# Optimization experiments

Measured on AMD Instinct MI355X. Metric: run time of the kernel, lower is better.

Reference implementation:

```python
import jax, jax.numpy as jnp
import numpy as np

V, E, H, D = 32000, 512, 512, 512  # vocab, emb_dim, enc_hid_dim, dec_hid_dim
B, S, T = 32, 64, 48               # batch, src_len, trg_len


def _gru_cell(x, h, Wih, Whh, bih, bhh):
    # PyTorch GRU cell semantics (gate order r, z, n)
    gi = x @ Wih.T + bih
    gh = h @ Whh.T + bhh
    ir, iz, i_n = jnp.split(gi, 3, axis=-1)
    hr, hz, h_n = jnp.split(gh, 3, axis=-1)
    r = jax.nn.sigmoid(ir + hr)
    z = jax.nn.sigmoid(iz + hz)
    n = jnp.tanh(i_n + r * h_n)
    return (1.0 - z) * n + z * h


def setup_inputs() -> dict:
    key = jax.random.key(0)
    ks = jax.random.split(key, 21)
    f = lambda k, shp: jax.random.normal(k, shp, dtype=jnp.float32) * 0.05
    inp = {
        'src': jax.random.randint(ks[0], (B, S), 0, V),
        'trg': jax.random.randint(ks[1], (T, B), 0, V),
        'emb': f(ks[2], (V, E)),
        'encf_Wih': f(ks[3], (3 * H, E)), 'encf_Whh': f(ks[4], (3 * H, H)),
        'encf_bih': f(ks[5], (3 * H,)), 'encf_bhh': f(ks[6], (3 * H,)),
        'encb_Wih': f(ks[7], (3 * H, E)), 'encb_Whh': f(ks[8], (3 * H, H)),
        'encb_bih': f(ks[9], (3 * H,)), 'encb_bhh': f(ks[10], (3 * H,)),
        'fc_W': f(ks[11], (D, 2 * H)), 'fc_b': f(ks[12], (D,)),
        'attn_W': f(ks[13], (D, D + 2 * H)), 'attn_v': f(ks[14], (D,)),
        'dec_Wih': f(ks[15], (3 * D, E + 2 * H)), 'dec_Whh': f(ks[16], (3 * D, D)),
        'dec_bih': f(ks[17], (3 * D,)), 'dec_bhh': f(ks[18], (3 * D,)),
        'out_W': f(ks[19], (V, 2 * H + D + E)),
        'out_b': jnp.zeros((V,), dtype=jnp.float32),
    }
    return inp


def _forward(src, trg, emb, encf_Wih, encf_Whh, encf_bih, encf_bhh,
             encb_Wih, encb_Whh, encb_bih, encb_bhh, fc_W, fc_b,
             attn_W, attn_v, dec_Wih, dec_Whh, dec_bih, dec_bhh, out_W, out_b):
    x = emb[src]                       # [B,S,E]
    xT = jnp.swapaxes(x, 0, 1)         # [S,B,E]
    h0 = jnp.zeros((src.shape[0], encf_Whh.shape[1]), dtype=x.dtype)

    def stepf(h, xt):
        h2 = _gru_cell(xt, h, encf_Wih, encf_Whh, encf_bih, encf_bhh)
        return h2, h2

    def stepb(h, xt):
        h2 = _gru_cell(xt, h, encb_Wih, encb_Whh, encb_bih, encb_bhh)
        return h2, h2

    hf, yf = jax.lax.scan(stepf, h0, xT)
    hb, yb = jax.lax.scan(stepb, h0, xT[::-1])
    # [B,S,2H] bidirectional encoder outputs (backward stream re-reversed)
    enc_out = jnp.concatenate([jnp.swapaxes(yf, 0, 1), jnp.swapaxes(yb[::-1], 0, 1)], axis=-1)
    # decoder init state from final fwd/bwd hidden
    s0 = jnp.tanh(jnp.concatenate([hf, hb], axis=-1) @ fc_W.T + fc_b)  # [B,D]

    def dec_step(s, tok):
        e = emb[tok]  # [B,E]
        srep = jnp.broadcast_to(s[:, None, :], (s.shape[0], enc_out.shape[1], s.shape[1]))
        energy = jnp.tanh(jnp.concatenate([srep, enc_out], axis=-1) @ attn_W.T)  # [B,S,D]
        a = jax.nn.softmax(energy @ attn_v, axis=1)  # [B,S]
        c = jnp.einsum('bs,bsh->bh', a, enc_out)     # [B,2H]
        s2 = _gru_cell(jnp.concatenate([e, c], axis=-1), s, dec_Wih, dec_Whh, dec_bih, dec_bhh)
        pred = jnp.concatenate([s2, c, e], axis=-1) @ out_W.T + out_b  # [B,V]
        return s2, pred

    # teacher forcing: decoder inputs are trg[0..T-2]
    _, preds = jax.lax.scan(dec_step, s0, trg[:-1])
    out0 = jnp.zeros((1,) + preds.shape[1:], dtype=preds.dtype)  # outputs[0] stays zero
    return jnp.concatenate([out0, preds], axis=0)  # [T,B,V]


def reference(src, trg, emb, encf_Wih, encf_Whh, encf_bih, encf_bhh,
              encb_Wih, encb_Whh, encb_bih, encb_bhh, fc_W, fc_b,
              attn_W, attn_v, dec_Wih, dec_Whh, dec_bih, dec_bhh, out_W, out_b):
    return _forward(src, trg, emb, encf_Wih, encf_Whh, encf_bih, encf_bhh,
                    encb_Wih, encb_Whh, encb_bih, encb_bhh, fc_W, fc_b,
                    attn_W, attn_v, dec_Wih, dec_Whh, dec_bih, dec_bhh, out_W, out_b)
```

## Files before the change

### kernel.cpp

```cpp
#include <hip/hip_runtime.h>
#include <stdint.h>
#include <stddef.h>

typedef __attribute__((ext_vector_type(8))) short short8;
typedef __attribute__((ext_vector_type(4))) float f32x4;

__device__ inline unsigned short f2bf(float f) {
  union { float f; uint32_t u; } v; v.f = f;
  uint32_t u = v.u;
  u += 0x7FFFu + ((u >> 16) & 1u);
  return (unsigned short)(u >> 16);
}
__device__ inline float bf2f(unsigned short h) {
  union { uint32_t u; float f; } v; v.u = ((uint32_t)h) << 16; return v.f;
}
__device__ inline short8 pack8(float4 a, float4 b) {
  short8 r;
  r[0] = (short)f2bf(a.x); r[1] = (short)f2bf(a.y);
  r[2] = (short)f2bf(a.z); r[3] = (short)f2bf(a.w);
  r[4] = (short)f2bf(b.x); r[5] = (short)f2bf(b.y);
  r[6] = (short)f2bf(b.z); r[7] = (short)f2bf(b.w);
  return r;
}
__device__ inline float tanh_fast(float x) {
  float xc = fminf(fmaxf(x, -9.f), 9.f);
  float e = __expf(2.f * xc);
  return (e - 1.f) * __builtin_amdgcn_rcpf(e + 1.f);
}
__device__ inline float sigm_fast(float x) {
  float xc = fminf(fmaxf(x, -30.f), 30.f);
  return __builtin_amdgcn_rcpf(1.f + __expf(-xc));
}

__global__ __launch_bounds__(128) void prep_gather(
    const int* __restrict__ src, const int* __restrict__ trg,
    const float* __restrict__ emb,
    unsigned short* __restrict__ xbf, unsigned short* __restrict__ ebf,
    unsigned short* __restrict__ Zbf) {
  int r = blockIdx.x, tid = threadIdx.x;
  if (r < 2048) {
    int b = r & 31, s = r >> 5;
    int tok = src[b * 64 + s];
    const float* e = emb + (size_t)tok * 512;
    float4 v = *(const float4*)(e + tid * 4);
    unsigned short* dst = xbf + (size_t)r * 512 + tid * 4;
    dst[0] = f2bf(v.x); dst[1] = f2bf(v.y); dst[2] = f2bf(v.z); dst[3] = f2bf(v.w);
  } else {
    int rr = r - 2048;
    int t = rr >> 5, b = rr & 31;
    unsigned short* dst = ebf + (size_t)rr * 512 + tid * 4;
    if (t < 47) {
      int tok = trg[t * 32 + b];
      const float* e = emb + (size_t)tok * 512;
      float4 v = *(const float4*)(e + tid * 4);
      unsigned short q0 = f2bf(v.x), q1 = f2bf(v.y), q2 = f2bf(v.z), q3 = f2bf(v.w);
      dst[0] = q0; dst[1] = q1; dst[2] = q2; dst[3] = q3;
      unsigned short* zd = Zbf + (size_t)rr * 2048 + 1536 + tid * 4;
      zd[0] = q0; zd[1] = q1; zd[2] = q2; zd[3] = q3;
    } else {
      dst[0] = 0; dst[1] = 0; dst[2] = 0; dst[3] = 0;
    }
  }
}

__global__ __launch_bounds__(256) void cvt_f32_bf16(const float* __restrict__ src,
                                                    unsigned short* __restrict__ dst,
                                                    long long n4) {
  long long i = (long long)blockIdx.x * 256 + threadIdx.x;
  long long stride = (long long)gridDim.x * 256;
  for (; i < n4; i += stride) {
    float4 v = ((const float4*)src)[i];
    unsigned short* d = dst + i * 4;
    d[0] = f2bf(v.x); d[1] = f2bf(v.y); d[2] = f2bf(v.z); d[3] = f2bf(v.w);
  }
}

__global__ __launch_bounds__(64) void cvt_rows(const float* __restrict__ src, int srcld,
                                               unsigned short* __restrict__ dst) {
  int r = blockIdx.x, c = threadIdx.x * 8;
  const float* s = src + (size_t)r * srcld + c;
  *(short8*)(dst + (size_t)r * 512 + c) = pack8(*(const float4*)s, *(const float4*)(s + 4));
}

template <bool ABF, bool BBF, bool WBF>
__global__ __launch_bounds__(256) void gemm_kernel(
    const void* __restrict__ Av, int lda,
    const void* __restrict__ Bv, int ldb, int bco,
    const float* __restrict__ bias,
    void* __restrict__ Cv, int ldc,
    int K, int Mvalid, int row_off) {
  __shared__ __align__(16) unsigned short As[128 * 32];
  __shared__ __align__(16) unsigned short Bs[128 * 32];
  const int tid = threadIdx.x;
  const int m0 = blockIdx.x * 128, n0 = blockIdx.y * 128;
  const int w = tid >> 6, lane = tid & 63;
  const int wm = w >> 1, wn = w & 1;
  const int fr = lane & 15, fq = lane >> 4;
  f32x4 acc[4][4];
#pragma unroll
  for (int mi = 0; mi < 4; ++mi)
#pragma unroll
    for (int ni = 0; ni < 4; ++ni) acc[mi][ni] = (f32x4){0.f, 0.f, 0.f, 0.f};
  for (int k0 = 0; k0 < K; k0 += 32) {
#pragma unroll
    for (int p = 0; p < 2; ++p) {
      int idx = p * 256 + tid;
      int row = idx >> 2, seg = idx & 3;
      if (ABF) {
        const unsigned short* Ab = (const unsigned short*)Av;
        *(short8*)(As + row * 32 + seg * 8) =
            *(const short8*)(Ab + (size_t)(m0 + row) * lda + k0 + seg * 8);
      } else {
        const float* Af = (const float*)Av;
        const float* ap = Af + (size_t)(m0 + row) * lda + k0 + seg * 8;
        *(short8*)(As + row * 32 + seg * 8) = pack8(*(const float4*)ap, *(const float4*)(ap + 4));
      }
      if (BBF) {
        const unsigned short* Bb = (const unsigned short*)Bv;
        *(short8*)(Bs + row * 32 + seg * 8) =
            *(const short8*)(Bb + (size_t)(n0 + row) * ldb + bco + k0 + seg * 8);
      } else {
        const float* Bf = (const float*)Bv;
        const float* bp = Bf + (size_t)(n0 + row) * ldb + bco + k0 + seg * 8;
        *(short8*)(Bs + row * 32 + seg * 8) = pack8(*(const float4*)bp, *(const float4*)(bp + 4));
      }
    }
    __syncthreads();
    short8 af[4], bfr[4];
#pragma unroll
    for (int mi = 0; mi < 4; ++mi)
      af[mi] = *(const short8*)(As + (wm * 64 + mi * 16 + fr) * 32 + fq * 8);
#pragma unroll
    for (int ni = 0; ni < 4; ++ni)
      bfr[ni] = *(const short8*)(Bs + (wn * 64 + ni * 16 + fr) * 32 + fq * 8);
#pragma unroll
    for (int mi = 0; mi < 4; ++mi)
#pragma unroll
      for (int ni = 0; ni < 4; ++ni)
        acc[mi][ni] = __builtin_amdgcn_mfma_f32_16x16x32_bf16(af[mi], bfr[ni], acc[mi][ni], 0, 0, 0);
    __syncthreads();
  }
#pragma unroll
  for (int mi = 0; mi < 4; ++mi)
#pragma unroll
    for (int ni = 0; ni < 4; ++ni) {
      int col = n0 + wn * 64 + ni * 16 + fr;
      float bv = bias ? bias[col] : 0.f;
#pragma unroll
      for (int j = 0; j < 4; ++j) {
        int rowm = m0 + wm * 64 + mi * 16 + fq * 4 + j;
        if (rowm < Mvalid) {
          float val = acc[mi][ni][j] + bv;
          if (WBF)
            ((unsigned short*)Cv)[(size_t)(rowm + row_off) * ldc + col] = f2bf(val);
          else
            ((float*)Cv)[(size_t)(rowm + row_off) * ldc + col] = val;
        }
      }
    }
}

__global__ __launch_bounds__(512) void enc_step(
    const float* __restrict__ Gif, const float* __restrict__ Gib,
    const unsigned short* __restrict__ whFbf, const unsigned short* __restrict__ whBbf,
    const float* __restrict__ bhhF, const float* __restrict__ bhhB,
    unsigned short* __restrict__ hbf,
    float* __restrict__ hf32,
    unsigned short* __restrict__ ebo,
    float* __restrict__ hcat,
    int t) {
  const int blk = blockIdx.x, tid = threadIdx.x;
  const int dir = blk >> 4, slice = blk & 15, D0 = slice * 32;
  const unsigned short* Wbf = dir ? whBbf : whFbf;
  const float* Gi = dir ? Gib : Gif;
  const float* bhh = dir ? bhhB : bhhF;
  __shared__ __align__(16) unsigned short hlds[32 * 520];
  __shared__ __align__(16) float gl[96 * 33];
  const unsigned short* hb = hbf + dir * 32768 + (t & 1) * 16384;
  for (int c = tid; c < 32 * 64; c += 512) {
    int r = c >> 6, seg = c & 63;
    *(short8*)(hlds + r * 520 + seg * 8) = *(const short8*)(hb + r * 512 + seg * 8);
  }
  __syncthreads();
  const int w = tid >> 6, lane = tid & 63, fr = lane & 15, fq = lane >> 4;
  if (w < 6) {
    int row = w * 16 + fr;
    int gr = (row >> 5) * 512 + D0 + (row & 31);
    const unsigned short* wrow = Wbf + (size_t)gr * 512;
    f32x4 acc0 = {0.f, 0.f, 0.f, 0.f}, acc1 = {0.f, 0.f, 0.f, 0.f};
#pragma unroll
    for (int k0 = 0; k0 < 512; k0 += 32) {
      short8 bq = *(const short8*)(wrow + k0 + fq * 8);
      short8 a0 = *(const short8*)(hlds + fr * 520 + k0 + fq * 8);
      short8 a1 = *(const short8*)(hlds + (16 + fr) * 520 + k0 + fq * 8);
      acc0 = __builtin_amdgcn_mfma_f32_16x16x32_bf16(a0, bq, acc0, 0, 0, 0);
      acc1 = __builtin_amdgcn_mfma_f32_16x16x32_bf16(a1, bq, acc1, 0, 0, 0);
    }
#pragma unroll
    for (int j = 0; j < 4; ++j) {
      gl[row * 33 + fq * 4 + j] = acc0[j];
      gl[row * 33 + 16 + fq * 4 + j] = acc1[j];
    }
  }
  __syncthreads();
  const int srow = dir ? 63 - t : t;
  unsigned short* hnb = hbf + dir * 32768 + ((t + 1) & 1) * 16384;
  const float* hcur = hf32 + dir * 32768 + (t & 1) * 16384;
  float* hnf = hf32 + dir * 32768 + ((t + 1) & 1) * 16384;
#pragma unroll
  for (int rep = 0; rep < 2; ++rep) {
    int idx = rep * 512 + tid, b = idx >> 5, dl = idx & 31, d = D0 + dl;
    float ar = gl[dl * 33 + b] + bhh[d];
    float az = gl[(32 + dl) * 33 + b] + bhh[512 + d];
    float an = gl[(64 + dl) * 33 + b] + bhh[1024 + d];
    const float* gi = Gi + ((size_t)srow * 32 + b) * 1536;
    float r = sigm_fast(gi[d] + ar);
    float z = sigm_fast(gi[512 + d] + az);
    float n = tanh_fast(gi[1024 + d] + r * an);
    float h2 = (1.f - z) * n + z * hcur[b * 512 + d];
    hnb[b * 512 + d] = f2bf(h2);
    hnf[b * 512 + d] = h2;
    ebo[((size_t)b * 64 + srow) * 1024 + (size_t)dir * 512 + d] = f2bf(h2);
    if (t == 63) hcat[(size_t)b * 1024 + (size_t)dir * 512 + d] = h2;
  }
}

__global__ __launch_bounds__(512) void tanh_s0(const float* __restrict__ s0raw,
                                               float* __restrict__ sf32,
                                               unsigned short* __restrict__ sbf) {
  int idx = blockIdx.x * 512 + threadIdx.x;
  float v = tanhf(s0raw[idx]);
  sf32[idx] = v;
  sbf[idx] = f2bf(v);
}

__global__ __launch_bounds__(512) void dec_proj(
    const unsigned short* __restrict__ Wcat, const float* __restrict__ decBhh,
    const unsigned short* __restrict__ sbf, float* __restrict__ gout, int t) {
  const int g = blockIdx.x, tid = threadIdx.x;
  __shared__ __align__(16) unsigned short slds[32 * 520];
  const unsigned short* sb = sbf + (t & 1) * 16384;
  for (int c = tid; c < 32 * 64; c += 512) {
    int r = c >> 6, seg = c & 63;
    *(short8*)(slds + r * 520 + seg * 8) = *(const short8*)(sb + r * 512 + seg * 8);
  }
  __syncthreads();
  const int w = tid >> 6, lane = tid & 63, fr = lane & 15, fq = lane >> 4;
  const int mt = w >> 2, nt = w & 3;
  int rc = g * 64 + nt * 16 + fr;
  const unsigned short* wrow = Wcat + (size_t)rc * 512;
  f32x4 acc = {0.f, 0.f, 0.f, 0.f};
#pragma unroll
  for (int k0 = 0; k0 < 512; k0 += 32) {
    short8 a = *(const short8*)(slds + (mt * 16 + fr) * 520 + k0 + fq * 8);
    short8 bq = *(const short8*)(wrow + k0 + fq * 8);
    acc = __builtin_amdgcn_mfma_f32_16x16x32_bf16(a, bq, acc, 0, 0, 0);
  }
  float bv = rc < 512 ? 0.f : decBhh[rc - 512];
#pragma unroll
  for (int j = 0; j < 4; ++j)
    gout[(size_t)(mt * 16 + fq * 4 + j) * 2048 + rc] = acc[j] + bv;
}

__global__ __launch_bounds__(512) void dec_attn(
    const float* __restrict__ attnV,
    const unsigned short* __restrict__ epf, const unsigned short* __restrict__ ebo,
    const unsigned short* __restrict__ EP2b, const float* __restrict__ Gie,
    const float* __restrict__ gout,
    unsigned short* __restrict__ sbf, float* __restrict__ sf32,
    unsigned short* __restrict__ Zbf, int t) {
  const int b = blockIdx.x, tid = threadIdx.x;
  __shared__ __align__(16) float gout_f[2048];
  __shared__ float raw[64], aaw[64];
  __shared__ float vlds[512];
  vlds[tid] = attnV[tid];
  *(float4*)(gout_f + tid * 4) = *(const float4*)(gout + (size_t)b * 2048 + tid * 4);
  __syncthreads();
  const int s_i = tid >> 3, l8 = tid & 7;
  {
    float part = 0.f;
    const float* gp = gout_f + l8 * 64;
    const unsigned short* ep = epf + ((size_t)b * 64 + s_i) * 512 + l8 * 64;
    const float* vv = vlds + l8 * 64;
#pragma unroll
    for (int jc = 0; jc < 8; ++jc) {
      short8 e8 = *(const short8*)(ep + jc * 8);
      float4 g0 = *(const float4*)(gp + jc * 8);
      float4 g1 = *(const float4*)(gp + jc * 8 + 4);
      float4 v0 = *(const float4*)(vv + jc * 8);
      float4 v1 = *(const float4*)(vv + jc * 8 + 4);
      part += tanh_fast(g0.x + bf2f((unsigned short)e8[0])) * v0.x;
      part += tanh_fast(g0.y + bf2f((unsigned short)e8[1])) * v0.y;
      part += tanh_fast(g0.z + bf2f((unsigned short)e8[2])) * v0.z;
      part += tanh_fast(g0.w + bf2f((unsigned short)e8[3])) * v0.w;
      part += tanh_fast(g1.x + bf2f((unsigned short)e8[4])) * v1.x;
      part += tanh_fast(g1.y + bf2f((unsigned short)e8[5])) * v1.y;
      part += tanh_fast(g1.z + bf2f((unsigned short)e8[6])) * v1.z;
      part += tanh_fast(g1.w + bf2f((unsigned short)e8[7])) * v1.w;
    }
    part += __shfl_xor(part, 1);
    part += __shfl_xor(part, 2);
    part += __shfl_xor(part, 4);
    if (l8 == 0) raw[s_i] = part;
  }
  __syncthreads();
  if (tid < 64) {
    float x = raw[tid];
    float m = x;
#pragma unroll
    for (int k = 1; k < 64; k <<= 1) m = fmaxf(m, __shfl_xor(m, k));
    float e = __expf(x - m);
    float s = e;
#pragma unroll
    for (int k = 1; k < 64; k <<= 1) s += __shfl_xor(s, k);
    aaw[tid] = e * __builtin_amdgcn_rcpf(s);
  }
  __syncthreads();
  float c0 = 0.f, c1 = 0.f, g0a = 0.f, g1a = 0.f, g2a = 0.f;
  {
    const unsigned short* eb = ebo + (size_t)b * 64 * 1024 + tid;
    const unsigned short* e2 = EP2b + (size_t)b * 64 * 1536 + tid;
#pragma unroll 8
    for (int s2 = 0; s2 < 64; ++s2) {
      float a = aaw[s2];
      c0 += a * bf2f(eb[(size_t)s2 * 1024]);
      c1 += a * bf2f(eb[(size_t)s2 * 1024 + 512]);
      g0a += a * bf2f(e2[(size_t)s2 * 1536]);
      g1a += a * bf2f(e2[(size_t)s2 * 1536 + 512]);
      g2a += a * bf2f(e2[(size_t)s2 * 1536 + 1024]);
    }
  }
  const float* gie = Gie + ((size_t)t * 32 + b) * 1536;
  float sprev = sf32[(t & 1) * 16384 + b * 512 + tid];
  float rr = sigm_fast(gie[tid] + g0a + gout_f[512 + tid]);
  float zz = sigm_fast(gie[512 + tid] + g1a + gout_f[1024 + tid]);
  float nn = tanh_fast(gie[1024 + tid] + g2a + rr * gout_f[1536 + tid]);
  float s2v = (1.f - zz) * nn + zz * sprev;
  sbf[((t + 1) & 1) * 16384 + b * 512 + tid] = f2bf(s2v);
  sf32[((t + 1) & 1) * 16384 + b * 512 + tid] = s2v;
  size_t zrow = ((size_t)t * 32 + b) * 2048;
  Zbf[zrow + tid] = f2bf(s2v);
  Zbf[zrow + 512 + tid] = f2bf(c0);
  Zbf[zrow + 1024 + tid] = f2bf(c1);
}

extern "C" void kernel_launch(void* const* d_in, const int* in_sizes, int n_in,
                              void* d_out, int out_size, void* d_ws, size_t ws_size,
                              hipStream_t stream) {
  (void)in_sizes; (void)n_in; (void)out_size;
  const int* src = (const int*)d_in[0];
  const int* trg = (const int*)d_in[1];
  const float* emb = (const float*)d_in[2];
  const float* encf_Wih = (const float*)d_in[3];
  const float* encf_Whh = (const float*)d_in[4];
  const float* encf_bih = (const float*)d_in[5];
  const float* encf_bhh = (const float*)d_in[6];
  const float* encb_Wih = (const float*)d_in[7];
  const float* encb_Whh = (const float*)d_in[8];
  const float* encb_bih = (const float*)d_in[9];
  const float* encb_bhh = (const float*)d_in[10];
  const float* fc_W = (const float*)d_in[11];
  const float* fc_b = (const float*)d_in[12];
  const float* attn_W = (const float*)d_in[13];
  const float* attn_v = (const float*)d_in[14];
  const float* dec_Wih = (const float*)d_in[15];
  const float* dec_Whh = (const float*)d_in[16];
  const float* dec_bih = (const float*)d_in[17];
  const float* dec_bhh = (const float*)d_in[18];
  const float* out_W = (const float*)d_in[19];
  const float* out_b = (const float*)d_in[20];
  float* out = (float*)d_out;

  char* p = (char*)d_ws;
  size_t off = 0;
  auto alloc = [&](size_t bytes) {
    void* r = p + off;
    off = (off + bytes + 255) & ~(size_t)255;
    return r;
  };
  unsigned short* xbf = (unsigned short*)alloc((size_t)2048 * 512 * 2);
  unsigned short* ebf = (unsigned short*)alloc((size_t)1536 * 512 * 2);
  unsigned short* Zbf = (unsigned short*)alloc((size_t)1536 * 2048 * 2);
  float* Gif = (float*)alloc((size_t)2048 * 1536 * 4);
  float* Gib = (float*)alloc((size_t)2048 * 1536 * 4);
  float* Gie = (float*)alloc((size_t)1536 * 1536 * 4);
  unsigned short* ebo = (unsigned short*)alloc((size_t)2048 * 1024 * 2);
  unsigned short* epf = (unsigned short*)alloc((size_t)2048 * 512 * 2);
  unsigned short* EP2b = (unsigned short*)alloc((size_t)2048 * 1536 * 2);
  unsigned short* whFbf = (unsigned short*)alloc((size_t)1536 * 512 * 2);
  unsigned short* whBbf = (unsigned short*)alloc((size_t)1536 * 512 * 2);
  unsigned short* Wcat = (unsigned short*)alloc((size_t)2048 * 512 * 2);
  unsigned short* hbf = (unsigned short*)alloc((size_t)2 * 2 * 32 * 512 * 2);
  float* hf32 = (float*)alloc((size_t)2 * 2 * 32 * 512 * 4);
  float* hcat = (float*)alloc((size_t)32 * 1024 * 4);
  float* s0raw = (float*)alloc((size_t)32 * 512 * 4);
  unsigned short* sbf = (unsigned short*)alloc((size_t)2 * 32 * 512 * 2);
  float* sf32 = (float*)alloc((size_t)2 * 32 * 512 * 4);
  float* gout = (float*)alloc((size_t)32 * 2048 * 4);
  unsigned short* outWbf = (unsigned short*)alloc((size_t)32000 * 2048 * 2);
  const bool bigB = (off <= ws_size);

  hipMemsetAsync(hbf, 0, (size_t)2 * 2 * 32 * 512 * 2, stream);
  hipMemsetAsync(hf32, 0, (size_t)2 * 2 * 32 * 512 * 4, stream);
  hipMemsetAsync(d_out, 0, (size_t)32 * 32000 * 4, stream);

  prep_gather<<<3584, 128, 0, stream>>>(src, trg, emb, xbf, ebf, Zbf);
  if (bigB)
    cvt_f32_bf16<<<4096, 256, 0, stream>>>(out_W, outWbf, (long long)32000 * 2048 / 4);
  cvt_rows<<<1536, 64, 0, stream>>>(encf_Whh, 512, whFbf);
  cvt_rows<<<1536, 64, 0, stream>>>(encb_Whh, 512, whBbf);
  cvt_rows<<<512, 64, 0, stream>>>(attn_W, 1536, Wcat);
  cvt_rows<<<1536, 64, 0, stream>>>(dec_Whh, 512, Wcat + (size_t)512 * 512);

  gemm_kernel<true, false, false><<<dim3(16, 12), 256, 0, stream>>>(
      xbf, 512, encf_Wih, 512, 0, encf_bih, Gif, 1536, 512, 2048, 0);
  gemm_kernel<true, false, false><<<dim3(16, 12), 256, 0, stream>>>(
      xbf, 512, encb_Wih, 512, 0, encb_bih, Gib, 1536, 512, 2048, 0);
  gemm_kernel<true, false, false><<<dim3(12, 12), 256, 0, stream>>>(
      ebf, 512, dec_Wih, 1536, 0, dec_bih, Gie, 1536, 512, 1536, 0);

  for (int t = 0; t < 64; ++t)
    enc_step<<<32, 512, 0, stream>>>(Gif, Gib, whFbf, whBbf, encf_bhh, encb_bhh,
                                     hbf, hf32, ebo, hcat, t);

  gemm_kernel<false, false, false><<<dim3(1, 4), 256, 0, stream>>>(
      hcat, 1024, fc_W, 1024, 0, fc_b, s0raw, 512, 1024, 32, 0);
  tanh_s0<<<32, 512, 0, stream>>>(s0raw, sf32, sbf);

  gemm_kernel<true, false, true><<<dim3(16, 4), 256, 0, stream>>>(
      ebo, 1024, attn_W, 1536, 512, nullptr, epf, 512, 1024, 2048, 0);
  gemm_kernel<true, false, true><<<dim3(16, 12), 256, 0, stream>>>(
      ebo, 1024, dec_Wih, 1536, 512, nullptr, EP2b, 1536, 1024, 2048, 0);

  for (int t = 0; t < 47; ++t) {
    dec_proj<<<32, 512, 0, stream>>>(Wcat, dec_bhh, sbf, gout, t);
    dec_attn<<<32, 512, 0, stream>>>(attn_v, epf, ebo, EP2b, Gie, gout,
                                     sbf, sf32, Zbf, t);
  }

  if (bigB)
    gemm_kernel<true, true, false><<<dim3(12, 250), 256, 0, stream>>>(
        Zbf, 2048, outWbf, 2048, 0, out_b, out, 32000, 2048, 1504, 32);
  else
    gemm_kernel<true, false, false><<<dim3(12, 250), 256, 0, stream>>>(
        Zbf, 2048, out_W, 2048, 0, out_b, out, 32000, 2048, 1504, 32);
}
```

Measured before the change: 2.004 ms.

## Overlap out_W bf16 conversion with encoder steps and add LDS-direct output GEMM

```diff
diff --git a/kernel.cpp b/kernel.cpp
--- a/kernel.cpp
+++ b/kernel.cpp
@@ -4,6 +4,7 @@
 
 typedef __attribute__((ext_vector_type(8))) short short8;
 typedef __attribute__((ext_vector_type(4))) float f32x4;
+typedef unsigned int u32;
 
 __device__ inline unsigned short f2bf(float f) {
   union { float f; uint32_t u; } v; v.f = f;
@@ -30,6 +31,11 @@
 __device__ inline float sigm_fast(float x) {
   float xc = fminf(fmaxf(x, -30.f), 30.f);
   return __builtin_amdgcn_rcpf(1.f + __expf(-xc));
+}
+__device__ inline void gl_lds16(const unsigned short* g, unsigned short* l) {
+  __builtin_amdgcn_global_load_lds(
+      (const __attribute__((address_space(1))) u32*)g,
+      (__attribute__((address_space(3))) u32*)l, 16, 0, 0);
 }
 
 __global__ __launch_bounds__(128) void prep_gather(
@@ -160,6 +166,63 @@
     }
 }
 
+__global__ __launch_bounds__(256) void gemm_big(
+    const unsigned short* __restrict__ A, int lda,
+    const unsigned short* __restrict__ B, int ldb,
+    const float* __restrict__ bias,
+    float* __restrict__ C, int ldc,
+    int K, int Mvalid, int row_off) {
+  __shared__ __align__(16) unsigned short As[128 * 32];
+  __shared__ __align__(16) unsigned short Bs[128 * 32];
+  const int tid = threadIdx.x;
+  int wg = blockIdx.x;
+  wg = (wg & 7) * 375 + (wg >> 3);
+  const int m0 = (wg % 12) * 128, n0 = (wg / 12) * 128;
+  const int w = tid >> 6, lane = tid & 63;
+  const int wm = w >> 1, wn = w & 1;
+  const int fr = lane & 15, fq = lane >> 4;
+  const int srow = lane >> 2, sseg = lane & 3;
+  f32x4 acc[4][4];
+#pragma unroll
+  for (int mi = 0; mi < 4; ++mi)
+#pragma unroll
+    for (int ni = 0; ni < 4; ++ni) acc[mi][ni] = (f32x4){0.f, 0.f, 0.f, 0.f};
+  for (int k0 = 0; k0 < K; k0 += 32) {
+#pragma unroll
+    for (int c = 0; c < 2; ++c) {
+      int row = w * 32 + c * 16 + srow;
+      gl_lds16(A + (size_t)(m0 + row) * lda + k0 + sseg * 8, As + row * 32);
+      gl_lds16(B + (size_t)(n0 + row) * ldb + k0 + sseg * 8, Bs + row * 32);
+    }
+    __syncthreads();
+    short8 af[4], bfr[4];
+#pragma unroll
+    for (int mi = 0; mi < 4; ++mi)
+      af[mi] = *(const short8*)(As + (wm * 64 + mi * 16 + fr) * 32 + fq * 8);
+#pragma unroll
+    for (int ni = 0; ni < 4; ++ni)
+      bfr[ni] = *(const short8*)(Bs + (wn * 64 + ni * 16 + fr) * 32 + fq * 8);
+#pragma unroll
+    for (int mi = 0; mi < 4; ++mi)
+#pragma unroll
+      for (int ni = 0; ni < 4; ++ni)
+        acc[mi][ni] = __builtin_amdgcn_mfma_f32_16x16x32_bf16(af[mi], bfr[ni], acc[mi][ni], 0, 0, 0);
+    __syncthreads();
+  }
+#pragma unroll
+  for (int mi = 0; mi < 4; ++mi)
+#pragma unroll
+    for (int ni = 0; ni < 4; ++ni) {
+      int col = n0 + wn * 64 + ni * 16 + fr;
+      float bv = bias[col];
+#pragma unroll
+      for (int j = 0; j < 4; ++j) {
+        int rowm = m0 + wm * 64 + mi * 16 + fq * 4 + j;
+        if (rowm < Mvalid) C[(size_t)(rowm + row_off) * ldc + col] = acc[mi][ni][j] + bv;
+      }
+    }
+}
+
 __global__ __launch_bounds__(512) void enc_step(
     const float* __restrict__ Gif, const float* __restrict__ Gib,
     const unsigned short* __restrict__ whFbf, const unsigned short* __restrict__ whBbf,
@@ -168,8 +231,20 @@
     float* __restrict__ hf32,
     unsigned short* __restrict__ ebo,
     float* __restrict__ hcat,
+    const float* __restrict__ outW, unsigned short* __restrict__ outWbf, int nCvt,
     int t) {
   const int blk = blockIdx.x, tid = threadIdx.x;
+  if (blk >= 32) {
+    if (blk - 32 < nCvt) {
+      size_t base4 = ((size_t)t * nCvt + (blk - 32)) * 1280;
+      for (int i = tid; i < 1280; i += 512) {
+        float4 v = ((const float4*)outW)[base4 + i];
+        unsigned short* d = outWbf + (base4 + i) * 4;
+        d[0] = f2bf(v.x); d[1] = f2bf(v.y); d[2] = f2bf(v.z); d[3] = f2bf(v.w);
+      }
+    }
+    return;
+  }
   const int dir = blk >> 4, slice = blk & 15, D0 = slice * 32;
   const unsigned short* Wbf = dir ? whBbf : whFbf;
   const float* Gi = dir ? Gib : Gif;
@@ -405,8 +480,6 @@
   hipMemsetAsync(d_out, 0, (size_t)32 * 32000 * 4, stream);
 
   prep_gather<<<3584, 128, 0, stream>>>(src, trg, emb, xbf, ebf, Zbf);
-  if (bigB)
-    cvt_f32_bf16<<<4096, 256, 0, stream>>>(out_W, outWbf, (long long)32000 * 2048 / 4);
   cvt_rows<<<1536, 64, 0, stream>>>(encf_Whh, 512, whFbf);
   cvt_rows<<<1536, 64, 0, stream>>>(encb_Whh, 512, whBbf);
   cvt_rows<<<512, 64, 0, stream>>>(attn_W, 1536, Wcat);
@@ -419,9 +492,10 @@
   gemm_kernel<true, false, false><<<dim3(12, 12), 256, 0, stream>>>(
       ebf, 512, dec_Wih, 1536, 0, dec_bih, Gie, 1536, 512, 1536, 0);
 
+  const int nCvt = bigB ? 200 : 0;
   for (int t = 0; t < 64; ++t)
-    enc_step<<<32, 512, 0, stream>>>(Gif, Gib, whFbf, whBbf, encf_bhh, encb_bhh,
-                                     hbf, hf32, ebo, hcat, t);
+    enc_step<<<32 + nCvt, 512, 0, stream>>>(Gif, Gib, whFbf, whBbf, encf_bhh, encb_bhh,
+                                            hbf, hf32, ebo, hcat, out_W, outWbf, nCvt, t);
 
   gemm_kernel<false, false, false><<<dim3(1, 4), 256, 0, stream>>>(
       hcat, 1024, fc_W, 1024, 0, fc_b, s0raw, 512, 1024, 32, 0);
@@ -439,8 +513,8 @@
   }
 
   if (bigB)
-    gemm_kernel<true, true, false><<<dim3(12, 250), 256, 0, stream>>>(
-        Zbf, 2048, outWbf, 2048, 0, out_b, out, 32000, 2048, 1504, 32);
+    gemm_big<<<3000, 256, 0, stream>>>(Zbf, 2048, outWbf, 2048, out_b,
+                                       out, 32000, 2048, 1504, 32);
   else
     gemm_kernel<true, false, false><<<dim3(12, 250), 256, 0, stream>>>(
         Zbf, 2048, out_W, 2048, 0, out_b, out, 32000, 2048, 1504, 32);
```

Result: no change. 1.982 ms (-1.1%).
